# Kernel optimization log

Hardware: AMD Instinct MI355X
Metric: run time of the kernel (lower is better)

The kernel has to match this reference:

```python
import jax, jax.numpy as jnp
import numpy as np

B, T, E, H = 64, 512, 512, 64
NEG_INF = jnp.float32(-1e30)


def setup_inputs() -> dict:
    key = jax.random.key(0)
    kx, kk, kq, kv = jax.random.split(key, 4)
    x = jax.random.normal(kx, (B, T, E), dtype=jnp.float32)
    attn_mask = jnp.ones((B, T), dtype=jnp.int32)
    Wk = jax.random.normal(kk, (E, H), dtype=jnp.float32) * (E ** -0.5)
    Wq = jax.random.normal(kq, (E, H), dtype=jnp.float32) * (E ** -0.5)
    Wv = jax.random.normal(kv, (E, H), dtype=jnp.float32) * (E ** -0.5)
    return {"x": x, "attn_mask": attn_mask, "Wk": Wk, "Wq": Wq, "Wv": Wv}


def reference(x, attn_mask, Wk, Wq, Wv):
    # x: (B,T,E); projections to (B,T,H)
    k = x @ Wk
    q = x @ Wq
    v = x @ Wv
    # scaled attention scores (B,T,T)
    wei = jnp.einsum('bth,bsh->bts', q, k) * (H ** -0.5)
    t = x.shape[1]
    causal = jnp.tril(jnp.ones((t, t), dtype=bool))  # (T,T)
    wei = jnp.where(causal[None, :, :], wei, NEG_INF)
    # padding mask: attn_mask (B,T) broadcast over query dim (matches unsqueeze(1).expand)
    wei = jnp.where(attn_mask[:, None, :] != 0, wei, NEG_INF)
    wei = jax.nn.softmax(wei, axis=-1)
    # dropout omitted (eval mode) for deterministic correctness baseline
    return jnp.einsum('bts,bsh->bth', wei, v)
```

## Files before the change

### kernel.cpp

```cpp
#include <hip/hip_runtime.h>

#define B 64
#define T 512
#define E 512
#define H 64
#define NEG_INF (-1e30f)

#define PBM 64
#define PBK 64
#define PN 192
#define NCHK (E / PBK)

#define QSCALE 0.18033688011112043f
#define DEFER_THR 8.0f

using short8 = __attribute__((ext_vector_type(8))) short;
using f32x16 = __attribute__((ext_vector_type(16))) float;

__device__ __forceinline__ unsigned short f2bf(float f) {
    unsigned int u = __float_as_uint(f);
    u += 0x7fffu + ((u >> 16) & 1u);
    return (unsigned short)(u >> 16);
}
__device__ __forceinline__ unsigned int bfpack_tr(float lo, float hi) {
    return (__float_as_uint(hi) & 0xffff0000u) | (__float_as_uint(lo) >> 16);
}
__device__ __forceinline__ void async_copy16(const void* g, void* l) {
    __builtin_amdgcn_global_load_lds(
        (const __attribute__((address_space(1))) unsigned int*)g,
        (__attribute__((address_space(3))) unsigned int*)l, 16, 0, 0);
}

__global__ __launch_bounds__(256) void prep(
    const float* __restrict__ Wq, const float* __restrict__ Wk,
    const float* __restrict__ Wv, const int* __restrict__ am,
    unsigned short* __restrict__ WT_swz, unsigned int* __restrict__ mbits)
{
    const int bid = blockIdx.x;
    if (bid < 384) {
        const int i = bid * 256 + threadIdx.x;
        const int c   = i / (PN * 64);
        const int rem = i - c * (PN * 64);
        const int row = rem >> 6;
        const int s   = rem & 63;
        const int klocal = s ^ ((row & 7) << 3);
        const int k   = c * 64 + klocal;
        const int seg = row >> 6, hh = row & 63;
        const float* W = (seg == 0) ? Wq : (seg == 1) ? Wk : Wv;
        WT_swz[i] = f2bf(W[(size_t)k * H + hh]);
    } else {
        const int i = (bid - 384) * 256 + threadIdx.x;
        const unsigned long long bal = __ballot(am[i] != 0);
        const int lane = threadIdx.x & 63;
        if (lane == 0)       mbits[i >> 5] = (unsigned int)bal;
        else if (lane == 32) mbits[i >> 5] = (unsigned int)(bal >> 32);
    }
}

__global__ __launch_bounds__(256) void proj_gemm(
    const float* __restrict__ x,
    const unsigned short* __restrict__ WT_swz,
    unsigned short* __restrict__ qfrag, unsigned short* __restrict__ kfrag,
    unsigned short* __restrict__ vfrag)
{
    __shared__ unsigned short Xs[2][PBM * 64];
    __shared__ unsigned short Ws[2][PN * 64];

    const int tid  = threadIdx.x;
    const int wid  = tid >> 6;
    const int lane = tid & 63;
    const int hi   = lane >> 5;
    const int r    = lane & 31;
    const int row0 = blockIdx.x * PBM;

    const int mrow  = (wid >> 1) * 32 + r;
    const int cbase = (wid & 1) * 96;

    const int aBase = mrow * 128;
    const int aXor  = (mrow & 7) << 4;
    int bBase[3], bXor[3];
    #pragma unroll
    for (int nt = 0; nt < 3; ++nt) {
        const int col = cbase + nt * 32 + r;
        bBase[nt] = col * 128;
        bXor[nt]  = (col & 7) << 4;
    }
    const int xs_rr[2]  = { tid >> 3, (256 + tid) >> 3 };
    const int xs_s16[2] = { tid & 7, tid & 7 };

    f32x16 acc[3] = {};

    {
        #pragma unroll
        for (int p = 0; p < 6; ++p) {
            const int u = p * 256 + wid * 64 + lane;
            async_copy16(WT_swz + u * 8, (char*)(&Ws[0][0]) + (p * 256 + wid * 64) * 16);
        }
        #pragma unroll
        for (int p = 0; p < 2; ++p) {
            const int rr = xs_rr[p], s16 = xs_s16[p];
            const float4* src = reinterpret_cast<const float4*>(
                &x[(size_t)(row0 + rr) * E + s16 * 8]);
            const float4 a0 = src[0], a1 = src[1];
            union { unsigned short us[8]; short8 v; } pk;
            pk.us[0] = f2bf(a0.x); pk.us[1] = f2bf(a0.y);
            pk.us[2] = f2bf(a0.z); pk.us[3] = f2bf(a0.w);
            pk.us[4] = f2bf(a1.x); pk.us[5] = f2bf(a1.y);
            pk.us[6] = f2bf(a1.z); pk.us[7] = f2bf(a1.w);
            const int cb = (s16 * 16) ^ ((rr & 7) << 4);
            *reinterpret_cast<short8*>((char*)(&Xs[0][0]) + rr * 128 + cb) = pk.v;
        }
        __syncthreads();
    }

    for (int c = 0; c < NCHK; ++c) {
        const int cur = c & 1;
        const bool pre = (c + 1 < NCHK);
        float4 xa[2], xb[2];

        if (pre) {
            const unsigned short* gw = WT_swz + (size_t)(c + 1) * (PN * 64);
            #pragma unroll
            for (int p = 0; p < 6; ++p) {
                const int u = p * 256 + wid * 64 + lane;
                async_copy16(gw + u * 8,
                             (char*)(&Ws[cur ^ 1][0]) + (p * 256 + wid * 64) * 16);
            }
            const int kc = (c + 1) * PBK;
            #pragma unroll
            for (int p = 0; p < 2; ++p) {
                const float4* src = reinterpret_cast<const float4*>(
                    &x[(size_t)(row0 + xs_rr[p]) * E + kc + xs_s16[p] * 8]);
                xa[p] = src[0];
                xb[p] = src[1];
            }
        }

        #pragma unroll
        for (int ks = 0; ks < 4; ++ks) {
            const int koff = ks * 32 + hi * 16;
            const short8 a = *reinterpret_cast<const short8*>(
                (const char*)(&Xs[cur][0]) + aBase + (koff ^ aXor));
            #pragma unroll
            for (int nt = 0; nt < 3; ++nt) {
                const short8 b = *reinterpret_cast<const short8*>(
                    (const char*)(&Ws[cur][0]) + bBase[nt] + (koff ^ bXor[nt]));
                acc[nt] = __builtin_amdgcn_mfma_f32_32x32x16_bf16(a, b, acc[nt], 0, 0, 0);
            }
        }

        if (pre) {
            #pragma unroll
            for (int p = 0; p < 2; ++p) {
                const int rr = xs_rr[p], s16 = xs_s16[p];
                union { unsigned short us[8]; short8 v; } pk;
                pk.us[0] = f2bf(xa[p].x); pk.us[1] = f2bf(xa[p].y);
                pk.us[2] = f2bf(xa[p].z); pk.us[3] = f2bf(xa[p].w);
                pk.us[4] = f2bf(xb[p].x); pk.us[5] = f2bf(xb[p].y);
                pk.us[6] = f2bf(xb[p].z); pk.us[7] = f2bf(xb[p].w);
                const int cb = (s16 * 16) ^ ((rr & 7) << 4);
                *reinterpret_cast<short8*>((char*)(&Xs[cur ^ 1][0]) + rr * 128 + cb) = pk.v;
            }
        }
        __syncthreads();
    }

    #pragma unroll
    for (int nt = 0; nt < 3; ++nt) {
        const int gc  = cbase + nt * 32 + r;
        const int seg = gc >> 6;
        const int h   = gc & 63;
        #pragma unroll
        for (int reg = 0; reg < 16; ++reg) {
            const int drow = (reg & 3) + 8 * (reg >> 2) + 4 * hi;
            const int grow = row0 + (wid >> 1) * 32 + drow;
            const float val = acc[nt][reg];
            const int bb  = grow >> 9;
            const int key = grow & 511;
            const int blk = key >> 5;
            const int kk  = key & 31;
            if (seg == 0) {
                qfrag[(((size_t)bb * 16 + blk) * 4 + (h >> 4)) * 512
                      + (((h >> 3) & 1) * 32 + kk) * 8 + (h & 7)] = f2bf(val * QSCALE);
            } else if (seg == 1) {
                kfrag[(((size_t)bb * 16 + blk) * 4 + (h >> 4)) * 512
                      + (((h >> 3) & 1) * 32 + kk) * 8 + (h & 7)] = f2bf(val);
            } else {
                vfrag[(((size_t)bb * 16 + blk) * 4 + ((kk >> 4) * 2 + (h >> 5))) * 512
                      + (((kk >> 3) & 1) * 32 + (h & 31)) * 8 + (kk & 7)] = f2bf(val);
            }
        }
    }
}

__global__ __launch_bounds__(256) void attn_online(
    const unsigned short* __restrict__ qfrag,
    const unsigned short* __restrict__ kfrag,
    const unsigned short* __restrict__ vfrag,
    const unsigned int* __restrict__ mbits,
    float* __restrict__ out)
{
    __shared__ float mlS[4][2][32];
    __shared__ float Ob[4][32][68];

    const int tid  = threadIdx.x;
    const int w    = tid >> 6;
    const int lane = tid & 63;
    const int hi = lane >> 5, r = lane & 31;
    const int h4 = 4 * hi;

    const int bid = blockIdx.x;
    const int kk2 = bid >> 3;
    const int b   = ((kk2 >> 4) << 3) | (bid & 7);
    const int s   = 15 - (kk2 & 15);
    const int t0  = s * 32;
    const int tq  = t0 + r;
    const int l8  = lane * 8;

    f32x16 accO[2] = {};
    float m = -INFINITY, l = 0.f;

    if (w <= s) {
        short8 qf[4];
        {
            const unsigned short* qb = qfrag + (((size_t)b * 16 + s) * 4) * 512;
            #pragma unroll
            for (int ks = 0; ks < 4; ++ks)
                qf[ks] = *reinterpret_cast<const short8*>(qb + ks * 512 + l8);
        }
        short8 kf[4], vb[4];
        {
            const unsigned short* kb = kfrag + (((size_t)b * 16 + w) * 4) * 512;
            const unsigned short* vv = vfrag + (((size_t)b * 16 + w) * 4) * 512;
            #pragma unroll
            for (int ks = 0; ks < 4; ++ks) {
                kf[ks] = *reinterpret_cast<const short8*>(kb + ks * 512 + l8);
                vb[ks] = *reinterpret_cast<const short8*>(vv + ks * 512 + l8);
            }
        }

        for (int j = w; j <= s; j += 4) {
            short8 kn[4], vn[4];
            if (j + 4 <= s) {
                const unsigned short* kb = kfrag + (((size_t)b * 16 + j + 4) * 4) * 512;
                const unsigned short* vv = vfrag + (((size_t)b * 16 + j + 4) * 4) * 512;
                #pragma unroll
                for (int ks = 0; ks < 4; ++ks) {
                    kn[ks] = *reinterpret_cast<const short8*>(kb + ks * 512 + l8);
                    vn[ks] = *reinterpret_cast<const short8*>(vv + ks * 512 + l8);
                }
            }

            f32x16 sc = {};
            #pragma unroll
            for (int ks = 0; ks < 4; ++ks)
                sc = __builtin_amdgcn_mfma_f32_32x32x16_bf16(kf[ks], qf[ks], sc, 0, 0, 0);

            const unsigned int mw = mbits[b * 16 + j];
            const bool fullm = (mw == 0xffffffffu);
            float cmax = -INFINITY;
            if (j == s) {
                #pragma unroll
                for (int reg = 0; reg < 16; ++reg) {
                    const int cr = (reg & 3) + 8 * (reg >> 2) + h4;
                    float v = sc[reg];
                    const bool bad = (32 * j + cr > tq) || (!fullm && !((mw >> cr) & 1u));
                    v = bad ? NEG_INF : v;
                    sc[reg] = v;
                    cmax = fmaxf(cmax, v);
                }
            } else if (fullm) {
                #pragma unroll
                for (int reg = 0; reg < 16; ++reg)
                    cmax = fmaxf(cmax, sc[reg]);
            } else {
                #pragma unroll
                for (int reg = 0; reg < 16; ++reg) {
                    const int cr = (reg & 3) + 8 * (reg >> 2) + h4;
                    float v = sc[reg];
                    v = ((mw >> cr) & 1u) ? v : NEG_INF;
                    sc[reg] = v;
                    cmax = fmaxf(cmax, v);
                }
            }
            cmax = fmaxf(cmax, __shfl_xor(cmax, 32));

            if (!__all(cmax <= m + DEFER_THR)) {
                const float m_new = fmaxf(m, cmax);
                const float scale = exp2f(m - m_new);
                f32x16 scf;
                #pragma unroll
                for (int reg = 0; reg < 16; ++reg)
                    scf[reg] = __shfl(scale, (reg & 3) + 8 * (reg >> 2) + h4);
                #pragma unroll
                for (int reg = 0; reg < 16; ++reg) {
                    accO[0][reg] *= scf[reg];
                    accO[1][reg] *= scf[reg];
                }
                l *= scale;
                m = m_new;
            }

            float csum = 0.f;
            #pragma unroll
            for (int reg = 0; reg < 16; ++reg) {
                const float p = exp2f(sc[reg] - m);
                sc[reg] = p;
                csum += p;
            }
            csum += __shfl_xor(csum, 32);
            l += csum;

            unsigned int pk[8];
            #pragma unroll
            for (int jj = 0; jj < 8; ++jj)
                pk[jj] = bfpack_tr(sc[2 * jj], sc[2 * jj + 1]);
            #pragma unroll
            for (int hs = 0; hs < 2; ++hs) {
                const unsigned int p01 = pk[hs * 4 + 0], p23 = pk[hs * 4 + 1];
                const unsigned int p45 = pk[hs * 4 + 2], p67 = pk[hs * 4 + 3];
                const unsigned int sendA = hi ? p01 : p45;
                const unsigned int sendB = hi ? p23 : p67;
                const unsigned int recvA = (unsigned int)__shfl_xor((int)sendA, 32);
                const unsigned int recvB = (unsigned int)__shfl_xor((int)sendB, 32);
                union { unsigned int uu[4]; short8 s8; } aw;
                aw.uu[0] = hi ? recvA : p01;
                aw.uu[1] = hi ? recvB : p23;
                aw.uu[2] = hi ? p45 : recvA;
                aw.uu[3] = hi ? p67 : recvB;
                #pragma unroll
                for (int tile = 0; tile < 2; ++tile)
                    accO[tile] = __builtin_amdgcn_mfma_f32_32x32x16_bf16(
                        aw.s8, vb[hs * 2 + tile], accO[tile], 0, 0, 0);
            }

            #pragma unroll
            for (int ks = 0; ks < 4; ++ks) { kf[ks] = kn[ks]; vb[ks] = vn[ks]; }
        }
    }

    if (hi == 0) { mlS[w][0][r] = m; mlS[w][1][r] = l; }
    #pragma unroll
    for (int reg = 0; reg < 16; ++reg) {
        const int qrow = (reg & 3) + 8 * (reg >> 2) + h4;
        Ob[w][qrow][r]      = accO[0][reg];
        Ob[w][qrow][r + 32] = accO[1][reg];
    }
    __syncthreads();

    {
        const int row = tid >> 3;
        const int c8  = (tid & 7) * 8;

        float mi[4], li[4];
        float mstar = -INFINITY;
        #pragma unroll
        for (int w2 = 0; w2 < 4; ++w2) {
            mi[w2] = mlS[w2][0][row];
            li[w2] = mlS[w2][1][row];
            mstar = fmaxf(mstar, mi[w2]);
        }
        float L = 0.f, fw[4];
        #pragma unroll
        for (int w2 = 0; w2 < 4; ++w2) {
            fw[w2] = exp2f(mi[w2] - mstar);
            L += fw[w2] * li[w2];
        }
        const float inv = 1.f / L;

        float acc[8] = {};
        #pragma unroll
        for (int w2 = 0; w2 < 4; ++w2) {
            const float4 lo = *reinterpret_cast<const float4*>(&Ob[w2][row][c8]);
            const float4 hi4v = *reinterpret_cast<const float4*>(&Ob[w2][row][c8 + 4]);
            acc[0] += fw[w2] * lo.x;  acc[1] += fw[w2] * lo.y;
            acc[2] += fw[w2] * lo.z;  acc[3] += fw[w2] * lo.w;
            acc[4] += fw[w2] * hi4v.x; acc[5] += fw[w2] * hi4v.y;
            acc[6] += fw[w2] * hi4v.z; acc[7] += fw[w2] * hi4v.w;
        }

        float* op = &out[((size_t)b * T + t0 + row) * H + c8];
        float4 o0 = { acc[0] * inv, acc[1] * inv, acc[2] * inv, acc[3] * inv };
        float4 o1 = { acc[4] * inv, acc[5] * inv, acc[6] * inv, acc[7] * inv };
        *reinterpret_cast<float4*>(op)     = o0;
        *reinterpret_cast<float4*>(op + 4) = o1;
    }
}

extern "C" void kernel_launch(void* const* d_in, const int* in_sizes, int n_in,
                              void* d_out, int out_size, void* d_ws, size_t ws_size,
                              hipStream_t stream) {
    const float* x         = (const float*)d_in[0];
    const int*   attn_mask = (const int*)d_in[1];
    const float* Wk        = (const float*)d_in[2];
    const float* Wq        = (const float*)d_in[3];
    const float* Wv        = (const float*)d_in[4];
    float* out = (float*)d_out;

    unsigned short* qfrag  = (unsigned short*)d_ws;
    unsigned short* kfrag  = qfrag + (size_t)B * T * H;
    unsigned short* vfrag  = kfrag + (size_t)B * T * H;
    unsigned short* WT_swz = vfrag + (size_t)B * T * H;
    unsigned int*   mbits  = (unsigned int*)(WT_swz + (size_t)PN * E);

    prep<<<512, 256, 0, stream>>>(Wq, Wk, Wv, attn_mask, WT_swz, mbits);
    proj_gemm<<<(B * T) / PBM, 256, 0, stream>>>(x, WT_swz, qfrag, kfrag, vfrag);
    attn_online<<<B * 16, 256, 0, stream>>>(qfrag, kfrag, vfrag, mbits, out);
}
```

Baseline: 48.13 us.

## Deepen projection GEMM pipeline with two-stage x prefetch and manual waitcnts

Restructures the projection GEMM main loop. The x global loads are now issued two chunks ahead in a register double buffer, and the loop is fully unrolled. The weight-tile async copies are regrouped so each wave-pair copies a contiguous half. __syncthreads is replaced by explicit vmcnt/lgkmcnt waits plus s_barrier, so outstanding global loads can stay in flight across the barrier. This is meant to hide global-load latency behind the MFMAs, at the cost of more registers and fragile hand-tuned wait counts.

```diff
diff --git a/kernel.cpp b/kernel.cpp
--- a/kernel.cpp
+++ b/kernel.cpp
@@ -30,6 +30,14 @@
         (const __attribute__((address_space(1))) unsigned int*)g,
         (__attribute__((address_space(3))) unsigned int*)l, 16, 0, 0);
 }
+
+#define WAIT_VM16() do { asm volatile("s_waitcnt vmcnt(16)" ::: "memory"); \
+                         __builtin_amdgcn_sched_barrier(0); } while (0)
+#define WAIT_VM0()  do { asm volatile("s_waitcnt vmcnt(0)"  ::: "memory"); \
+                         __builtin_amdgcn_sched_barrier(0); } while (0)
+#define LGKM_BARRIER() do { asm volatile("s_waitcnt lgkmcnt(0)" ::: "memory"); \
+                            __builtin_amdgcn_s_barrier(); \
+                            __builtin_amdgcn_sched_barrier(0); } while (0)
 
 __global__ __launch_bounds__(256) void prep(
     const float* __restrict__ Wq, const float* __restrict__ Wk,
@@ -74,7 +82,8 @@
     const int row0 = blockIdx.x * PBM;
 
     const int mrow  = (wid >> 1) * 32 + r;
-    const int cbase = (wid & 1) * 96;
+    const int hhalf = wid & 1;
+    const int cbase = hhalf * 96;
 
     const int aBase = mrow * 128;
     const int aXor  = (mrow & 7) << 4;
@@ -86,55 +95,65 @@
         bXor[nt]  = (col & 7) << 4;
     }
     const int xs_rr[2]  = { tid >> 3, (256 + tid) >> 3 };
-    const int xs_s16[2] = { tid & 7, tid & 7 };
+    const int xs_s16    = tid & 7;
+
+    const unsigned short* wsrcbase = WT_swz + hhalf * 6144 + lane * 8;
+    const int wdst = hhalf * 12288;
 
     f32x16 acc[3] = {};
+    float4 xA[2][2], xB[2][2];
 
     {
         #pragma unroll
-        for (int p = 0; p < 6; ++p) {
-            const int u = p * 256 + wid * 64 + lane;
-            async_copy16(WT_swz + u * 8, (char*)(&Ws[0][0]) + (p * 256 + wid * 64) * 16);
-        }
+        for (int p = 0; p < 12; ++p)
+            async_copy16(wsrcbase + p * 512,
+                         (char*)(&Ws[0][0]) + wdst + p * 1024);
         #pragma unroll
         for (int p = 0; p < 2; ++p) {
-            const int rr = xs_rr[p], s16 = xs_s16[p];
             const float4* src = reinterpret_cast<const float4*>(
-                &x[(size_t)(row0 + rr) * E + s16 * 8]);
+                &x[(size_t)(row0 + xs_rr[p]) * E + xs_s16 * 8]);
             const float4 a0 = src[0], a1 = src[1];
             union { unsigned short us[8]; short8 v; } pk;
             pk.us[0] = f2bf(a0.x); pk.us[1] = f2bf(a0.y);
             pk.us[2] = f2bf(a0.z); pk.us[3] = f2bf(a0.w);
             pk.us[4] = f2bf(a1.x); pk.us[5] = f2bf(a1.y);
             pk.us[6] = f2bf(a1.z); pk.us[7] = f2bf(a1.w);
-            const int cb = (s16 * 16) ^ ((rr & 7) << 4);
-            *reinterpret_cast<short8*>((char*)(&Xs[0][0]) + rr * 128 + cb) = pk.v;
-        }
-        __syncthreads();
-    }
-
+            const int cb = (xs_s16 * 16) ^ ((xs_rr[p] & 7) << 4);
+            *reinterpret_cast<short8*>((char*)(&Xs[0][0]) + xs_rr[p] * 128 + cb) = pk.v;
+        }
+        #pragma unroll
+        for (int p = 0; p < 2; ++p) {
+            const float4* src = reinterpret_cast<const float4*>(
+                &x[(size_t)(row0 + xs_rr[p]) * E + PBK + xs_s16 * 8]);
+            xA[1][p] = src[0];
+            xB[1][p] = src[1];
+        }
+        LGKM_BARRIER();
+    }
+
+    #pragma unroll
     for (int c = 0; c < NCHK; ++c) {
         const int cur = c & 1;
-        const bool pre = (c + 1 < NCHK);
-        float4 xa[2], xb[2];
-
-        if (pre) {
-            const unsigned short* gw = WT_swz + (size_t)(c + 1) * (PN * 64);
-            #pragma unroll
-            for (int p = 0; p < 6; ++p) {
-                const int u = p * 256 + wid * 64 + lane;
-                async_copy16(gw + u * 8,
-                             (char*)(&Ws[cur ^ 1][0]) + (p * 256 + wid * 64) * 16);
-            }
-            const int kc = (c + 1) * PBK;
+
+        if (c + 1 < NCHK) {
+            const unsigned short* gw = wsrcbase + (size_t)(c + 1) * (PN * 64);
+            #pragma unroll
+            for (int p = 0; p < 12; ++p)
+                async_copy16(gw + p * 512,
+                             (char*)(&Ws[cur ^ 1][0]) + wdst + p * 1024);
+        }
+        if (c + 2 < NCHK) {
+            const int kc = (c + 2) * PBK;
             #pragma unroll
             for (int p = 0; p < 2; ++p) {
                 const float4* src = reinterpret_cast<const float4*>(
-                    &x[(size_t)(row0 + xs_rr[p]) * E + kc + xs_s16[p] * 8]);
-                xa[p] = src[0];
-                xb[p] = src[1];
-            }
-        }
+                    &x[(size_t)(row0 + xs_rr[p]) * E + kc + xs_s16 * 8]);
+                xA[cur][p] = src[0];
+                xB[cur][p] = src[1];
+            }
+        }
+
+        if (c == NCHK - 1) { WAIT_VM0(); } else { WAIT_VM16(); }
 
         #pragma unroll
         for (int ks = 0; ks < 4; ++ks) {
@@ -149,20 +168,21 @@
             }
         }
 
-        if (pre) {
+        if (c + 1 < NCHK) {
+            const int nb = (c + 1) & 1;
             #pragma unroll
             for (int p = 0; p < 2; ++p) {
-                const int rr = xs_rr[p], s16 = xs_s16[p];
                 union { unsigned short us[8]; short8 v; } pk;
-                pk.us[0] = f2bf(xa[p].x); pk.us[1] = f2bf(xa[p].y);
-                pk.us[2] = f2bf(xa[p].z); pk.us[3] = f2bf(xa[p].w);
-                pk.us[4] = f2bf(xb[p].x); pk.us[5] = f2bf(xb[p].y);
-                pk.us[6] = f2bf(xb[p].z); pk.us[7] = f2bf(xb[p].w);
-                const int cb = (s16 * 16) ^ ((rr & 7) << 4);
-                *reinterpret_cast<short8*>((char*)(&Xs[cur ^ 1][0]) + rr * 128 + cb) = pk.v;
-            }
-        }
-        __syncthreads();
+                pk.us[0] = f2bf(xA[nb][p].x); pk.us[1] = f2bf(xA[nb][p].y);
+                pk.us[2] = f2bf(xA[nb][p].z); pk.us[3] = f2bf(xA[nb][p].w);
+                pk.us[4] = f2bf(xB[nb][p].x); pk.us[5] = f2bf(xB[nb][p].y);
+                pk.us[6] = f2bf(xB[nb][p].z); pk.us[7] = f2bf(xB[nb][p].w);
+                const int cb = (xs_s16 * 16) ^ ((xs_rr[p] & 7) << 4);
+                *reinterpret_cast<short8*>(
+                    (char*)(&Xs[cur ^ 1][0]) + xs_rr[p] * 128 + cb) = pk.v;
+            }
+            LGKM_BARRIER();
+        }
     }
 
     #pragma unroll
```

Measured after the change: 45.27 us. -5.9%, faster.

## Restructure projection GEMM: full X tile in LDS, weights in registers

Applied to the files above, without the earlier changes.

The projection kernel now loads the whole 64x512 X tile into LDS once, using a rotation swizzle. Each of six waves keeps its 32-column weight slice in registers, loaded directly from an MFMA-fragment layout that prep builds and that now folds the Q scale into Wq. This removes the double-buffered K-loop with its per-chunk barriers and weight LDS staging. The cost is 64 KB of LDS, heavy register use, and less overlap of global loads with MFMA. The attention kernel also raises wave priority around its MFMA sections.

```diff
diff --git a/kernel.cpp b/kernel.cpp
--- a/kernel.cpp
+++ b/kernel.cpp
@@ -7,9 +7,7 @@
 #define NEG_INF (-1e30f)
 
 #define PBM 64
-#define PBK 64
 #define PN 192
-#define NCHK (E / PBK)
 
 #define QSCALE 0.18033688011112043f
 #define DEFER_THR 8.0f
@@ -25,29 +23,29 @@
 __device__ __forceinline__ unsigned int bfpack_tr(float lo, float hi) {
     return (__float_as_uint(hi) & 0xffff0000u) | (__float_as_uint(lo) >> 16);
 }
-__device__ __forceinline__ void async_copy16(const void* g, void* l) {
-    __builtin_amdgcn_global_load_lds(
-        (const __attribute__((address_space(1))) unsigned int*)g,
-        (__attribute__((address_space(3))) unsigned int*)l, 16, 0, 0);
-}
 
 __global__ __launch_bounds__(256) void prep(
     const float* __restrict__ Wq, const float* __restrict__ Wk,
     const float* __restrict__ Wv, const int* __restrict__ am,
-    unsigned short* __restrict__ WT_swz, unsigned int* __restrict__ mbits)
+    unsigned short* __restrict__ wfrag, unsigned int* __restrict__ mbits)
 {
     const int bid = blockIdx.x;
     if (bid < 384) {
-        const int i = bid * 256 + threadIdx.x;
-        const int c   = i / (PN * 64);
-        const int rem = i - c * (PN * 64);
-        const int row = rem >> 6;
-        const int s   = rem & 63;
-        const int klocal = s ^ ((row & 7) << 3);
-        const int k   = c * 64 + klocal;
-        const int seg = row >> 6, hh = row & 63;
+        const int i  = bid * 256 + threadIdx.x;
+        const int f  = i >> 9;
+        const int le = i & 511;
+        const int ln = le >> 3, e = le & 7;
+        const int ko = ln >> 5, rr = ln & 31;
+        const int c  = f / 24;
+        const int ks = (f - c * 24) / 6;
+        const int ct = f % 6;
+        const int col = ct * 32 + rr;
+        const int kk  = c * 64 + ks * 16 + ko * 8 + e;
+        const int seg = col >> 6, hh = col & 63;
         const float* W = (seg == 0) ? Wq : (seg == 1) ? Wk : Wv;
-        WT_swz[i] = f2bf(W[(size_t)k * H + hh]);
+        float v = W[(size_t)kk * H + hh];
+        if (seg == 0) v *= QSCALE;
+        wfrag[i] = f2bf(v);
     } else {
         const int i = (bid - 384) * 256 + threadIdx.x;
         const unsigned long long bal = __ballot(am[i] != 0);
@@ -57,131 +55,124 @@
     }
 }
 
-__global__ __launch_bounds__(256) void proj_gemm(
+__global__ __launch_bounds__(384, 3) void proj_gemm(
     const float* __restrict__ x,
-    const unsigned short* __restrict__ WT_swz,
+    const unsigned short* __restrict__ wfrag,
     unsigned short* __restrict__ qfrag, unsigned short* __restrict__ kfrag,
     unsigned short* __restrict__ vfrag)
 {
-    __shared__ unsigned short Xs[2][PBM * 64];
-    __shared__ unsigned short Ws[2][PN * 64];
+    __shared__ unsigned short Xs[PBM * 512];
 
     const int tid  = threadIdx.x;
-    const int wid  = tid >> 6;
+    const int w    = tid >> 6;
     const int lane = tid & 63;
     const int hi   = lane >> 5;
     const int r    = lane & 31;
     const int row0 = blockIdx.x * PBM;
 
-    const int mrow  = (wid >> 1) * 32 + r;
-    const int cbase = (wid & 1) * 96;
-
-    const int aBase = mrow * 128;
-    const int aXor  = (mrow & 7) << 4;
-    int bBase[3], bXor[3];
-    #pragma unroll
-    for (int nt = 0; nt < 3; ++nt) {
-        const int col = cbase + nt * 32 + r;
-        bBase[nt] = col * 128;
-        bXor[nt]  = (col & 7) << 4;
-    }
-    const int xs_rr[2]  = { tid >> 3, (256 + tid) >> 3 };
-    const int xs_s16[2] = { tid & 7, tid & 7 };
-
-    f32x16 acc[3] = {};
-
     {
-        #pragma unroll
-        for (int p = 0; p < 6; ++p) {
-            const int u = p * 256 + wid * 64 + lane;
-            async_copy16(WT_swz + u * 8, (char*)(&Ws[0][0]) + (p * 256 + wid * 64) * 16);
-        }
-        #pragma unroll
-        for (int p = 0; p < 2; ++p) {
-            const int rr = xs_rr[p], s16 = xs_s16[p];
-            const float4* src = reinterpret_cast<const float4*>(
-                &x[(size_t)(row0 + rr) * E + s16 * 8]);
-            const float4 a0 = src[0], a1 = src[1];
-            union { unsigned short us[8]; short8 v; } pk;
-            pk.us[0] = f2bf(a0.x); pk.us[1] = f2bf(a0.y);
-            pk.us[2] = f2bf(a0.z); pk.us[3] = f2bf(a0.w);
-            pk.us[4] = f2bf(a1.x); pk.us[5] = f2bf(a1.y);
-            pk.us[6] = f2bf(a1.z); pk.us[7] = f2bf(a1.w);
-            const int cb = (s16 * 16) ^ ((rr & 7) << 4);
-            *reinterpret_cast<short8*>((char*)(&Xs[0][0]) + rr * 128 + cb) = pk.v;
-        }
-        __syncthreads();
-    }
-
-    for (int c = 0; c < NCHK; ++c) {
-        const int cur = c & 1;
-        const bool pre = (c + 1 < NCHK);
-        float4 xa[2], xb[2];
-
-        if (pre) {
-            const unsigned short* gw = WT_swz + (size_t)(c + 1) * (PN * 64);
-            #pragma unroll
-            for (int p = 0; p < 6; ++p) {
-                const int u = p * 256 + wid * 64 + lane;
-                async_copy16(gw + u * 8,
-                             (char*)(&Ws[cur ^ 1][0]) + (p * 256 + wid * 64) * 16);
-            }
-            const int kc = (c + 1) * PBK;
-            #pragma unroll
-            for (int p = 0; p < 2; ++p) {
-                const float4* src = reinterpret_cast<const float4*>(
-                    &x[(size_t)(row0 + xs_rr[p]) * E + kc + xs_s16[p] * 8]);
-                xa[p] = src[0];
-                xb[p] = src[1];
-            }
-        }
-
-        #pragma unroll
-        for (int ks = 0; ks < 4; ++ks) {
-            const int koff = ks * 32 + hi * 16;
-            const short8 a = *reinterpret_cast<const short8*>(
-                (const char*)(&Xs[cur][0]) + aBase + (koff ^ aXor));
-            #pragma unroll
-            for (int nt = 0; nt < 3; ++nt) {
-                const short8 b = *reinterpret_cast<const short8*>(
-                    (const char*)(&Ws[cur][0]) + bBase[nt] + (koff ^ bXor[nt]));
-                acc[nt] = __builtin_amdgcn_mfma_f32_32x32x16_bf16(a, b, acc[nt], 0, 0, 0);
-            }
-        }
-
-        if (pre) {
-            #pragma unroll
-            for (int p = 0; p < 2; ++p) {
-                const int rr = xs_rr[p], s16 = xs_s16[p];
+        float4 A[13], Bq[13];
+        #pragma unroll
+        for (int d = 0; d < 2; ++d) {
+            const int i = d * 384 + tid;
+            if (i < 4096) {
+                const float4* s = reinterpret_cast<const float4*>(
+                    &x[(size_t)(row0 + (i >> 6)) * E + (i & 63) * 8]);
+                A[d] = s[0]; Bq[d] = s[1];
+            }
+        }
+        #pragma unroll
+        for (int st = 0; st < 11; ++st) {
+            if (st + 2 < 11) {
+                const int i = (st + 2) * 384 + tid;
+                if (i < 4096) {
+                    const float4* s = reinterpret_cast<const float4*>(
+                        &x[(size_t)(row0 + (i >> 6)) * E + (i & 63) * 8]);
+                    A[st + 2] = s[0]; Bq[st + 2] = s[1];
+                }
+            }
+            const int i = st * 384 + tid;
+            if (i < 4096) {
+                const int rr = i >> 6, g = i & 63;
                 union { unsigned short us[8]; short8 v; } pk;
-                pk.us[0] = f2bf(xa[p].x); pk.us[1] = f2bf(xa[p].y);
-                pk.us[2] = f2bf(xa[p].z); pk.us[3] = f2bf(xa[p].w);
-                pk.us[4] = f2bf(xb[p].x); pk.us[5] = f2bf(xb[p].y);
-                pk.us[6] = f2bf(xb[p].z); pk.us[7] = f2bf(xb[p].w);
-                const int cb = (s16 * 16) ^ ((rr & 7) << 4);
-                *reinterpret_cast<short8*>((char*)(&Xs[cur ^ 1][0]) + rr * 128 + cb) = pk.v;
-            }
-        }
-        __syncthreads();
-    }
-
-    #pragma unroll
-    for (int nt = 0; nt < 3; ++nt) {
-        const int gc  = cbase + nt * 32 + r;
-        const int seg = gc >> 6;
-        const int h   = gc & 63;
+                pk.us[0] = f2bf(A[st].x);  pk.us[1] = f2bf(A[st].y);
+                pk.us[2] = f2bf(A[st].z);  pk.us[3] = f2bf(A[st].w);
+                pk.us[4] = f2bf(Bq[st].x); pk.us[5] = f2bf(Bq[st].y);
+                pk.us[6] = f2bf(Bq[st].z); pk.us[7] = f2bf(Bq[st].w);
+                *reinterpret_cast<short8*>(
+                    (char*)Xs + rr * 1024 + ((g + rr) & 63) * 16) = pk.v;
+            }
+        }
+    }
+
+    short8 breg[16];
+    #pragma unroll
+    for (int c = 0; c < 4; ++c)
+        #pragma unroll
+        for (int ks = 0; ks < 4; ++ks)
+            breg[c * 4 + ks] = *reinterpret_cast<const short8*>(
+                wfrag + ((size_t)((c * 4 + ks) * 6 + w)) * 512 + lane * 8);
+
+    __syncthreads();
+
+    f32x16 acc[2] = {};
+
+    #pragma unroll
+    for (int c = 0; c < 4; ++c) {
+        #pragma unroll
+        for (int mt = 0; mt < 2; ++mt) {
+            const int mrow = mt * 32 + r;
+            #pragma unroll
+            for (int ks = 0; ks < 4; ++ks) {
+                const int g = c * 8 + ks * 2 + hi;
+                const short8 a = *reinterpret_cast<const short8*>(
+                    (const char*)Xs + mrow * 1024 + ((g + mrow) & 63) * 16);
+                acc[mt] = __builtin_amdgcn_mfma_f32_32x32x16_bf16(
+                    a, breg[c * 4 + ks], acc[mt], 0, 0, 0);
+            }
+        }
+    }
+
+    #pragma unroll
+    for (int c = 0; c < 4; ++c)
+        #pragma unroll
+        for (int ks = 0; ks < 4; ++ks)
+            breg[c * 4 + ks] = *reinterpret_cast<const short8*>(
+                wfrag + ((size_t)(((c + 4) * 4 + ks) * 6 + w)) * 512 + lane * 8);
+
+    #pragma unroll
+    for (int c = 0; c < 4; ++c) {
+        #pragma unroll
+        for (int mt = 0; mt < 2; ++mt) {
+            const int mrow = mt * 32 + r;
+            #pragma unroll
+            for (int ks = 0; ks < 4; ++ks) {
+                const int g = (c + 4) * 8 + ks * 2 + hi;
+                const short8 a = *reinterpret_cast<const short8*>(
+                    (const char*)Xs + mrow * 1024 + ((g + mrow) & 63) * 16);
+                acc[mt] = __builtin_amdgcn_mfma_f32_32x32x16_bf16(
+                    a, breg[c * 4 + ks], acc[mt], 0, 0, 0);
+            }
+        }
+    }
+
+    const int gc  = w * 32 + r;
+    const int seg = gc >> 6;
+    const int h   = gc & 63;
+    #pragma unroll
+    for (int mt = 0; mt < 2; ++mt) {
         #pragma unroll
         for (int reg = 0; reg < 16; ++reg) {
             const int drow = (reg & 3) + 8 * (reg >> 2) + 4 * hi;
-            const int grow = row0 + (wid >> 1) * 32 + drow;
-            const float val = acc[nt][reg];
+            const int grow = row0 + mt * 32 + drow;
+            const float val = acc[mt][reg];
             const int bb  = grow >> 9;
             const int key = grow & 511;
             const int blk = key >> 5;
             const int kk  = key & 31;
             if (seg == 0) {
                 qfrag[(((size_t)bb * 16 + blk) * 4 + (h >> 4)) * 512
-                      + (((h >> 3) & 1) * 32 + kk) * 8 + (h & 7)] = f2bf(val * QSCALE);
+                      + (((h >> 3) & 1) * 32 + kk) * 8 + (h & 7)] = f2bf(val);
             } else if (seg == 1) {
                 kfrag[(((size_t)bb * 16 + blk) * 4 + (h >> 4)) * 512
                       + (((h >> 3) & 1) * 32 + kk) * 8 + (h & 7)] = f2bf(val);
@@ -251,10 +242,12 @@
                 }
             }
 
+            __builtin_amdgcn_s_setprio(1);
             f32x16 sc = {};
             #pragma unroll
             for (int ks = 0; ks < 4; ++ks)
                 sc = __builtin_amdgcn_mfma_f32_32x32x16_bf16(kf[ks], qf[ks], sc, 0, 0, 0);
+            __builtin_amdgcn_s_setprio(0);
 
             const unsigned int mw = mbits[b * 16 + j];
             const bool fullm = (mw == 0xffffffffu);
@@ -315,6 +308,7 @@
             #pragma unroll
             for (int jj = 0; jj < 8; ++jj)
                 pk[jj] = bfpack_tr(sc[2 * jj], sc[2 * jj + 1]);
+            __builtin_amdgcn_s_setprio(1);
             #pragma unroll
             for (int hs = 0; hs < 2; ++hs) {
                 const unsigned int p01 = pk[hs * 4 + 0], p23 = pk[hs * 4 + 1];
@@ -333,6 +327,7 @@
                     accO[tile] = __builtin_amdgcn_mfma_f32_32x32x16_bf16(
                         aw.s8, vb[hs * 2 + tile], accO[tile], 0, 0, 0);
             }
+            __builtin_amdgcn_s_setprio(0);
 
             #pragma unroll
             for (int ks = 0; ks < 4; ++ks) { kf[ks] = kn[ks]; vb[ks] = vn[ks]; }
@@ -397,13 +392,13 @@
     const float* Wv        = (const float*)d_in[4];
     float* out = (float*)d_out;
 
-    unsigned short* qfrag  = (unsigned short*)d_ws;
-    unsigned short* kfrag  = qfrag + (size_t)B * T * H;
-    unsigned short* vfrag  = kfrag + (size_t)B * T * H;
-    unsigned short* WT_swz = vfrag + (size_t)B * T * H;
-    unsigned int*   mbits  = (unsigned int*)(WT_swz + (size_t)PN * E);
-
-    prep<<<512, 256, 0, stream>>>(Wq, Wk, Wv, attn_mask, WT_swz, mbits);
-    proj_gemm<<<(B * T) / PBM, 256, 0, stream>>>(x, WT_swz, qfrag, kfrag, vfrag);
+    unsigned short* qfrag = (unsigned short*)d_ws;
+    unsigned short* kfrag = qfrag + (size_t)B * T * H;
+    unsigned short* vfrag = kfrag + (size_t)B * T * H;
+    unsigned short* wfrag = vfrag + (size_t)B * T * H;
+    unsigned int*   mbits = (unsigned int*)(wfrag + (size_t)PN * E);
+
+    prep<<<512, 256, 0, stream>>>(Wq, Wk, Wv, attn_mask, wfrag, mbits);
+    proj_gemm<<<(B * T) / PBM, 384, 0, stream>>>(x, wfrag, qfrag, kfrag, vfrag);
     attn_online<<<B * 16, 256, 0, stream>>>(qfrag, kfrag, vfrag, mbits, out);
 }
```

Result: slower. 49.30 us (+2.4%).
